# Kernel tuning notes

Hardware: AMD Instinct MI355X
Metric: run time of the kernel (lower is better)

The kernel has to match this reference:

```python
import jax, jax.numpy as jnp
import numpy as np

N = 2048          # natoms
NBINS = 100
R_START = 0.0
R_END = 7.5       # cutoff = r_range[1]
BOX = 20.0        # cubic cell edge (diagonal cell)
CUTOFF_B = R_END + 0.5  # cutoff_boundary used by generate_nbr_list


def setup_inputs() -> dict:
    key = jax.random.key(0)
    xyz = jax.random.uniform(key, (N, 3), dtype=jnp.float32) * BOX
    cell = jnp.full((3,), BOX, dtype=jnp.float32)
    # rdf buffers: bins = linspace(start, end, nbins+1); smear offsets = linspace(start, end, nbins)
    bins = jnp.linspace(R_START, R_END, NBINS + 1, dtype=jnp.float32)
    offsets = jnp.linspace(R_START, R_END, NBINS, dtype=jnp.float32)
    return {"xyz": xyz, "cell": cell, "bins": bins, "offsets": offsets}


def reference(xyz, cell, bins, offsets):
    # ---- generate_nbr_list: all-pairs displacement with minimum-image PBC ----
    disp = xyz[None, :, :] - xyz[:, None, :]                       # [N, N, 3]
    shift = (-(disp >= 0.5 * cell).astype(disp.dtype)
             + (disp < -0.5 * cell).astype(disp.dtype))
    disp = disp + shift * cell                                      # wrapped displacement
    dsq = jnp.sum(disp * disp, axis=-1)                             # [N, N]
    # pairs within cutoff_boundary, excluding self (dsq == 0)
    mask = (dsq < CUTOFF_B * CUTOFF_B) & (dsq != 0.0)
    dist = jnp.sqrt(jnp.where(mask, dsq, 1.0))                      # safe sqrt off-mask

    # ---- GaussianSmearing (width = bin spacing, coeff = -0.5/width^2) ----
    width = offsets[1] - offsets[0]
    coeff = -0.5 / (width * width)
    diff = dist[..., None] - offsets                                # [N, N, NBINS]
    g = jnp.exp(coeff * diff * diff)

    # masked sum over all pairs == gather-then-sum of the torch version
    count = jnp.sum(g * mask[..., None].astype(g.dtype), axis=(0, 1))  # [NBINS]
    count = count / jnp.sum(count)

    # ---- normalization to g(r) ----
    vol_bins = 4.0 * np.pi / 3.0 * (bins[1:] ** 3 - bins[:-1] ** 3)
    V = 4.0 / 3.0 * np.pi * R_END ** 3
    rdf_out = count / (vol_bins / V)
    return count, bins, rdf_out
```

## Files before the change

### kernel.cpp

```cpp
#include <hip/hip_runtime.h>
#include <hip/hip_bf16.h>


#define N_ATOMS 2048
#define HALF    1024
#define NBINS   100
#define S_FINE  17
#define FBINS   1744
#define NCOPY   4
#define TAPS    103
#define NDIR    12
#define TLOW    8.0f
#define NBLOCKS 256
#define NTHREADS 1024
#define ROWS_PB 8
#define PADB    112
#define NSUB    16
#define TSTRIDE 64

__global__ __launch_bounds__(1024) void rdf_fused(
    const float* __restrict__ xyz,
    const float* __restrict__ cell,
    const float* __restrict__ offsets,
    const float* __restrict__ bins,
    float* __restrict__ out,
    float* __restrict__ partials,
    unsigned* __restrict__ tickets)
{
    __shared__ unsigned fine[NCOPY][FBINS];
    __shared__ float wtab[TAPS];
    __shared__ float conv[NBINS][8];
    __shared__ float cd[16];
    __shared__ float ssum[2];
    __shared__ unsigned stick;

    const int tid = threadIdx.x;
    const int bid = blockIdx.x;

    for (int a = tid; a < NCOPY * FBINS; a += NTHREADS)
        (&fine[0][0])[a] = 0u;
    if (tid < 16)   cd[tid] = 0.0f;
    if (tid < TAPS) {
        const float u = ((float)tid - 50.5f) * (1.0f / (float)S_FINE);
        wtab[tid] = __expf(-0.5f * u * u);
    }
    __syncthreads();

    const float cx = cell[0], cy = cell[1], cz = cell[2];
    const float hcx = 0.5f * cx, hcy = 0.5f * cy, hcz = 0.5f * cz;

    const float width = offsets[1] - offsets[0];
    const float invw  = 1.0f / width;
    const float cutd   = 102.5f * width;
    const float cut2   = cutd * cutd;

    unsigned* const myfine = fine[tid >> 8];

    const int row0 = bid << 3;
    #pragma unroll
    for (int r = 0; r < ROWS_PB; ++r) {
        const int i = row0 + r;
        const float xi = xyz[3 * i + 0];
        const float yi = xyz[3 * i + 1];
        const float zi = xyz[3 * i + 2];
        if (tid == HALF - 1 && i >= HALF) continue;
        const int j = (i + 1 + tid) & (N_ATOMS - 1);

        float dx = xyz[3 * j + 0] - xi;
        float dy = xyz[3 * j + 1] - yi;
        float dz = xyz[3 * j + 2] - zi;
        dx += (dx >= hcx) ? -cx : ((dx < -hcx) ? cx : 0.0f);
        dy += (dy >= hcy) ? -cy : ((dy < -hcy) ? cy : 0.0f);
        dz += (dz >= hcz) ? -cz : ((dz < -hcz) ? cz : 0.0f);

        const float dsq = dx * dx + dy * dy + dz * dz;
        if (dsq < cut2 && dsq != 0.0f) {
            const float tu = sqrtf(dsq) * invw;
            if (tu >= TLOW) {
                atomicAdd(&myfine[(int)(tu * (float)S_FINE)], 1u);
            } else {
                int khi = (int)tu + 4; if (khi > NDIR - 1) khi = NDIR - 1;
                for (int k = 0; k <= khi; ++k) {
                    const float e = tu - (float)k;
                    atomicAdd(&cd[k], __expf(-0.5f * e * e));
                }
            }
        }
    }

    __syncthreads();

    for (int a = tid; a < FBINS; a += NTHREADS)
        fine[0][a] += fine[1][a] + fine[2][a] + fine[3][a];
    __syncthreads();

    if (tid < 400) {
        const int k = tid >> 2;
        const int c = tid & 3;
        const int m0 = c * 26;
        const int mcnt = (c == 3) ? 25 : 26;
        float s = 0.0f;
        for (int mm = 0; mm < mcnt; ++mm) {
            const int m = m0 + mm;
            const int f = S_FINE * k + m - 51;
            if (f >= 0) s += wtab[m] * (float)fine[0][f];
        }
        conv[k][c] = s;
    }
    __syncthreads();

    if (tid < NBINS) {
        float raw = conv[tid][0] + conv[tid][1] + conv[tid][2] + conv[tid][3];
        if (tid < NDIR) raw += cd[tid];
        float old = atomicExch(&partials[bid * PADB + tid], raw);
        asm volatile("" :: "v"(old));
    }

    __syncthreads();
    if (tid == 0) {
        unsigned last = 0u;
        const unsigned so = __hip_atomic_fetch_add(
            &tickets[(bid & (NSUB - 1)) * TSTRIDE], 1u,
            __ATOMIC_RELAXED, __HIP_MEMORY_SCOPE_AGENT);
        if ((so & (NBLOCKS / NSUB - 1)) == (NBLOCKS / NSUB - 1)) {
            const unsigned mo = __hip_atomic_fetch_add(
                &tickets[NSUB * TSTRIDE], 1u,
                __ATOMIC_RELAXED, __HIP_MEMORY_SCOPE_AGENT);
            last = ((mo & (NSUB - 1)) == (NSUB - 1)) ? 1u : 0u;
        }
        if (last) {
            __hip_atomic_fetch_add(&tickets[NSUB * TSTRIDE], 0u,
                                   __ATOMIC_ACQUIRE, __HIP_MEMORY_SCOPE_AGENT);
        }
        stick = last;
    }
    __syncthreads();
    if (!stick) return;

    {
        const int b = tid & 127;
        const int c = tid >> 7;
        if (b < NBINS) {
            float s = 0.0f;
            #pragma unroll 8
            for (int q = 0; q < NBLOCKS / 8; ++q) {
                const int blk = c * (NBLOCKS / 8) + q;
                s += __hip_atomic_load(&partials[blk * PADB + b],
                                       __ATOMIC_RELAXED,
                                       __HIP_MEMORY_SCOPE_SYSTEM);
            }
            conv[b][c] = s;
        }
    }
    __syncthreads();

    float raw = 0.0f;
    if (tid < NBINS) {
        #pragma unroll
        for (int c = 0; c < 8; ++c) raw += conv[tid][c];
    }
    if (tid < 128) {
        float v = raw;
        #pragma unroll
        for (int o = 32; o > 0; o >>= 1) v += __shfl_down(v, o);
        if ((tid & 63) == 0) ssum[tid >> 6] = v;
    }
    __syncthreads();
    const float S = ssum[0] + ssum[1];

    if (tid < NBINS) {
        const float cnt = raw / S;
        out[tid] = cnt;
        const float b0 = bins[tid], b1 = bins[tid + 1];
        const float R  = bins[NBINS];
        out[201 + tid] = cnt * (R * R * R) / (b1 * b1 * b1 - b0 * b0 * b0);
    }
    if (tid < NBINS + 1) {
        out[100 + tid] = bins[tid];
    }
}

extern "C" void kernel_launch(void* const* d_in, const int* in_sizes, int n_in,
                              void* d_out, int out_size, void* d_ws, size_t ws_size,
                              hipStream_t stream) {
    const float* xyz     = (const float*)d_in[0];
    const float* cell    = (const float*)d_in[1];
    const float* bins    = (const float*)d_in[2];
    const float* offsets = (const float*)d_in[3];
    float* out = (float*)d_out;

    float*    partials = (float*)d_ws;
    unsigned* tickets  = (unsigned*)((char*)d_ws +
                                     (size_t)NBLOCKS * PADB * sizeof(float));

    rdf_fused<<<NBLOCKS, NTHREADS, 0, stream>>>(xyz, cell, offsets, bins, out,
                                                partials, tickets);
}
```

Baseline: 15.13 us.

## Replace flat last-block reduction with two-level hierarchical group reduction

```diff
diff --git a/kernel.cpp b/kernel.cpp
--- a/kernel.cpp
+++ b/kernel.cpp
@@ -16,7 +16,11 @@
 #define ROWS_PB 8
 #define PADB    112
 #define NSUB    16
+#define GSZ     16
 #define TSTRIDE 64
+#define TICK_OFF  (NBLOCKS * PADB * 4)
+#define TICK_BYTES ((NSUB * TSTRIDE + 1) * 4)
+#define L2_OFF    (TICK_OFF + 8192)
 
 __global__ __launch_bounds__(1024) void rdf_fused(
     const float* __restrict__ xyz,
@@ -25,7 +29,8 @@
     const float* __restrict__ bins,
     float* __restrict__ out,
     float* __restrict__ partials,
-    unsigned* __restrict__ tickets)
+    unsigned* __restrict__ tickets,
+    float* __restrict__ l2)
 {
     __shared__ unsigned fine[NCOPY][FBINS];
     __shared__ float wtab[TAPS];
@@ -117,22 +122,17 @@
     }
 
     __syncthreads();
+    const int g = bid >> 4;
     if (tid == 0) {
-        unsigned last = 0u;
         const unsigned so = __hip_atomic_fetch_add(
-            &tickets[(bid & (NSUB - 1)) * TSTRIDE], 1u,
+            &tickets[g * TSTRIDE], 1u,
             __ATOMIC_RELAXED, __HIP_MEMORY_SCOPE_AGENT);
-        if ((so & (NBLOCKS / NSUB - 1)) == (NBLOCKS / NSUB - 1)) {
-            const unsigned mo = __hip_atomic_fetch_add(
-                &tickets[NSUB * TSTRIDE], 1u,
-                __ATOMIC_RELAXED, __HIP_MEMORY_SCOPE_AGENT);
-            last = ((mo & (NSUB - 1)) == (NSUB - 1)) ? 1u : 0u;
-        }
-        if (last) {
-            __hip_atomic_fetch_add(&tickets[NSUB * TSTRIDE], 0u,
+        unsigned subwin = (so == GSZ - 1) ? 1u : 0u;
+        if (subwin) {
+            __hip_atomic_fetch_add(&tickets[g * TSTRIDE], 0u,
                                    __ATOMIC_ACQUIRE, __HIP_MEMORY_SCOPE_AGENT);
         }
-        stick = last;
+        stick = subwin;
     }
     __syncthreads();
     if (!stick) return;
@@ -142,10 +142,50 @@
         const int c = tid >> 7;
         if (b < NBINS) {
             float s = 0.0f;
-            #pragma unroll 8
-            for (int q = 0; q < NBLOCKS / 8; ++q) {
-                const int blk = c * (NBLOCKS / 8) + q;
+            #pragma unroll
+            for (int qq = 0; qq < 2; ++qq) {
+                const int blk = (g << 4) + (c << 1) + qq;
                 s += __hip_atomic_load(&partials[blk * PADB + b],
+                                       __ATOMIC_RELAXED,
+                                       __HIP_MEMORY_SCOPE_SYSTEM);
+            }
+            conv[b][c] = s;
+        }
+    }
+    __syncthreads();
+
+    if (tid < NBINS) {
+        float s = 0.0f;
+        #pragma unroll
+        for (int c = 0; c < 8; ++c) s += conv[tid][c];
+        float old = atomicExch(&l2[g * PADB + tid], s);
+        asm volatile("" :: "v"(old));
+    }
+
+    __syncthreads();
+    if (tid == 0) {
+        const unsigned mo = __hip_atomic_fetch_add(
+            &tickets[NSUB * TSTRIDE], 1u,
+            __ATOMIC_RELAXED, __HIP_MEMORY_SCOPE_AGENT);
+        unsigned last = (mo == NSUB - 1) ? 1u : 0u;
+        if (last) {
+            __hip_atomic_fetch_add(&tickets[NSUB * TSTRIDE], 0u,
+                                   __ATOMIC_ACQUIRE, __HIP_MEMORY_SCOPE_AGENT);
+        }
+        stick = last;
+    }
+    __syncthreads();
+    if (!stick) return;
+
+    {
+        const int b = tid & 127;
+        const int c = tid >> 7;
+        if (b < NBINS) {
+            float s = 0.0f;
+            #pragma unroll
+            for (int qq = 0; qq < 2; ++qq) {
+                const int g2 = (c << 1) + qq;
+                s += __hip_atomic_load(&l2[g2 * PADB + b],
                                        __ATOMIC_RELAXED,
                                        __HIP_MEMORY_SCOPE_SYSTEM);
             }
@@ -190,9 +230,10 @@
     float* out = (float*)d_out;
 
     float*    partials = (float*)d_ws;
-    unsigned* tickets  = (unsigned*)((char*)d_ws +
-                                     (size_t)NBLOCKS * PADB * sizeof(float));
-
+    unsigned* tickets  = (unsigned*)((char*)d_ws + TICK_OFF);
+    float*    l2       = (float*)((char*)d_ws + L2_OFF);
+
+    hipMemsetAsync(tickets, 0, TICK_BYTES, stream);
     rdf_fused<<<NBLOCKS, NTHREADS, 0, stream>>>(xyz, cell, offsets, bins, out,
-                                                partials, tickets);
+                                                partials, tickets, l2);
 }
```

Result: slower. 23.11 us (+52.7%).
